# Performance work log

Hardware: AMD Instinct MI355X
Metric: run time of the kernel (lower is better)

## Reference

```python
import jax, jax.numpy as jnp
import numpy as np

D_MODEL, Q, V, H = 1024, 64, 64, 16
B, K = 2, 2048


def setup_inputs() -> dict:
    key = jax.random.key(0)
    ks = jax.random.split(key, 8)
    s = 0.02
    return {
        "xi": jax.random.normal(ks[0], (B, K, D_MODEL), dtype=jnp.float32),
        # stacked per-head projection weights (equivalent to h separate nn.Linear)
        "Wq": jax.random.normal(ks[1], (H, D_MODEL, Q), dtype=jnp.float32) * s,
        "bq": jax.random.normal(ks[2], (H, Q), dtype=jnp.float32) * s,
        "Wk": jax.random.normal(ks[3], (H, D_MODEL, Q), dtype=jnp.float32) * s,
        "bk": jax.random.normal(ks[4], (H, Q), dtype=jnp.float32) * s,
        "Wv": jax.random.normal(ks[5], (H, D_MODEL, V), dtype=jnp.float32) * s,
        "bv": jax.random.normal(ks[6], (H, V), dtype=jnp.float32) * s,
        "Wo": jax.random.normal(ks[7], (H * V, D_MODEL), dtype=jnp.float32) * s,
        "bo": jnp.zeros((D_MODEL,), dtype=jnp.float32),
    }


def reference(xi, Wq, bq, Wk, bk, Wv, bv, Wo, bo):
    # per-head projections, batched over heads: [B,H,K,q]
    queries = jnp.einsum("bkd,hdq->bhkq", xi, Wq) + bq[None, :, None, :]
    keys = jnp.einsum("bkd,hdq->bhkq", xi, Wk) + bk[None, :, None, :]
    values = jnp.einsum("bkd,hdv->bhkv", xi, Wv) + bv[None, :, None, :]
    # NOTE: original scales by sqrt(queries.shape[1]) == sqrt(seq_len K), not sqrt(q)
    scale = 1.0 / np.sqrt(xi.shape[1]).astype(np.float32)
    scores = jax.nn.softmax(jnp.einsum("bhkq,bhmq->bhkm", queries, keys) * scale, axis=-1)
    attn = jnp.einsum("bhkm,bhmv->bhkv", scores, values)  # [B,H,K,v]
    # concat heads along last dim -> [B,K,H*v]
    attn = attn.transpose(0, 2, 1, 3).reshape(xi.shape[0], xi.shape[1], -1)
    return attn @ Wo + bo
```

## Files before the change

kernel.cpp:

```cpp
#include <hip/hip_runtime.h>
#include <math.h>

typedef __bf16 bf16x8 __attribute__((ext_vector_type(8)));
typedef float  f32x4  __attribute__((ext_vector_type(4)));
typedef float  f32x16 __attribute__((ext_vector_type(16)));
typedef unsigned short u16x8 __attribute__((ext_vector_type(8)));

#define D_MODEL 1024
#define QDIM    64
#define HEADS   16
#define BATCH   2
#define SEQ     2048
#define M_ROWS  (BATCH*SEQ)
#define NCAT    (HEADS*3*QDIM)

__device__ __forceinline__ unsigned short f2bf(float f) {
    unsigned int u = __float_as_uint(f);
    u += 0x7fffu + ((u >> 16) & 1u);
    return (unsigned short)(u >> 16);
}

__device__ __forceinline__ void gl16(const unsigned short* g, unsigned short* l) {
    __builtin_amdgcn_global_load_lds(
        (const __attribute__((address_space(1))) unsigned int*)g,
        (__attribute__((address_space(3))) unsigned int*)l, 16, 0, 0);
}

__global__ __launch_bounds__(256) void k_cvt_bf16(const float* __restrict__ in,
                                                  unsigned short* __restrict__ out) {
    int i = (blockIdx.x * 256 + threadIdx.x) * 8;
    f32x4 a = *(const f32x4*)(in + i);
    f32x4 b = *(const f32x4*)(in + i + 4);
    u16x8 o;
    o[0]=f2bf(a[0]); o[1]=f2bf(a[1]); o[2]=f2bf(a[2]); o[3]=f2bf(a[3]);
    o[4]=f2bf(b[0]); o[5]=f2bf(b[1]); o[6]=f2bf(b[2]); o[7]=f2bf(b[3]);
    *(u16x8*)(out + i) = o;
}

__global__ __launch_bounds__(256) void k_prep_wcat(const float* __restrict__ Wq,
                                                   const float* __restrict__ Wk,
                                                   const float* __restrict__ Wv,
                                                   const float* __restrict__ bq,
                                                   const float* __restrict__ bk,
                                                   const float* __restrict__ bv,
                                                   unsigned short* __restrict__ WcatT,
                                                   float* __restrict__ bcat,
                                                   float qscale) {
    int blk = blockIdx.x;
    int dt = blk & 15, h = (blk >> 4) & 15, s = blk >> 8;
    const float* W = (s == 0) ? Wq : (s == 1) ? Wk : Wv;
    float sc = (s == 0) ? qscale : 1.0f;
    __shared__ float t[64][65];
    int tid = threadIdx.x;
    int dr = tid >> 2, qc = (tid & 3) * 16;
    const float* src = W + (size_t)h * (D_MODEL * QDIM) + (size_t)(dt * 64 + dr) * QDIM + qc;
#pragma unroll
    for (int j = 0; j < 4; ++j) {
        f32x4 v = *(const f32x4*)(src + j * 4);
        t[dr][qc + j * 4 + 0] = v[0]; t[dr][qc + j * 4 + 1] = v[1];
        t[dr][qc + j * 4 + 2] = v[2]; t[dr][qc + j * 4 + 3] = v[3];
    }
    __syncthreads();
    int q = tid >> 2, dc = (tid & 3) * 16;
    unsigned short* dst = WcatT + (size_t)(h * 192 + s * 64 + q) * D_MODEL + dt * 64 + dc;
#pragma unroll
    for (int j = 0; j < 2; ++j) {
        u16x8 o;
#pragma unroll
        for (int e = 0; e < 8; ++e) o[e] = f2bf(t[dc + j * 8 + e][q] * sc);
        *(u16x8*)(dst + j * 8) = o;
    }
    if (dt == 0 && tid < 64) {
        const float* bb = (s == 0) ? bq : (s == 1) ? bk : bv;
        bcat[h * 192 + s * 64 + tid] = bb[h * QDIM + tid] * sc;
    }
}

__global__ __launch_bounds__(256) void k_prep_wo(const float* __restrict__ Wo,
                                                 unsigned short* __restrict__ WoT) {
    int blk = blockIdx.x;
    int ct = blk & 15, rt = blk >> 4;
    __shared__ float t[64][65];
    int tid = threadIdx.x;
    int dr = tid >> 2, qc = (tid & 3) * 16;
    const float* src = Wo + (size_t)(rt * 64 + dr) * D_MODEL + ct * 64 + qc;
#pragma unroll
    for (int j = 0; j < 4; ++j) {
        f32x4 v = *(const f32x4*)(src + j * 4);
        t[dr][qc + j * 4 + 0] = v[0]; t[dr][qc + j * 4 + 1] = v[1];
        t[dr][qc + j * 4 + 2] = v[2]; t[dr][qc + j * 4 + 3] = v[3];
    }
    __syncthreads();
    int q = tid >> 2, dc = (tid & 3) * 16;
    unsigned short* dst = WoT + (size_t)(ct * 64 + q) * D_MODEL + rt * 64 + dc;
#pragma unroll
    for (int j = 0; j < 2; ++j) {
        u16x8 o;
#pragma unroll
        for (int e = 0; e < 8; ++e) o[e] = f2bf(t[dc + j * 8 + e][q]);
        *(u16x8*)(dst + j * 8) = o;
    }
}

template<bool OUT_BF16>
__global__ __launch_bounds__(256) void k_gemm(const unsigned short* __restrict__ A,
                                              const unsigned short* __restrict__ BT,
                                              const float* __restrict__ bias,
                                              void* __restrict__ Cout,
                                              int N, int Kd) {
    __shared__ __align__(16) unsigned short Alds[128 * 64];
    __shared__ __align__(16) unsigned short Blds[128 * 64];
    const int tid = threadIdx.x;
    const int lane = tid & 63, w = tid >> 6;
    const int g = lane >> 4, c = lane & 15;
    int nwg = gridDim.x * gridDim.y;
    int bid = blockIdx.y * gridDim.x + blockIdx.x;
    int sw = (bid & 7) * (nwg >> 3) + (bid >> 3);
    int bx = sw % gridDim.x, by = sw / gridDim.x;
    const int m0 = by * 128, n0 = bx * 128;
    const int wm = (w >> 1) * 64, wn = (w & 1) * 64;
    const int r8 = lane >> 3, chx = (lane & 7) ^ r8;
    const int swz = c & 7;
    f32x4 acc[4][4] = {};

    for (int k0 = 0; k0 < Kd; k0 += 64) {
        __builtin_amdgcn_sched_barrier(0);
        __builtin_amdgcn_s_barrier();
#pragma unroll
        for (int i = 0; i < 4; ++i) {
            int row = w * 32 + i * 8 + r8;
            gl16(A + (size_t)(m0 + row) * Kd + k0 + chx * 8, Alds + w * 2048 + i * 512);
            gl16(BT + (size_t)(n0 + row) * Kd + k0 + chx * 8, Blds + w * 2048 + i * 512);
        }
        asm volatile("s_waitcnt vmcnt(0)" ::: "memory");
        __builtin_amdgcn_s_barrier();
        __builtin_amdgcn_sched_barrier(0);
#pragma unroll
        for (int kk = 0; kk < 2; ++kk) {
            bf16x8 af[4], bfr[4];
#pragma unroll
            for (int mf = 0; mf < 4; ++mf) {
                int row = wm + mf * 16 + c;
                af[mf] = *(const bf16x8*)(Alds + row * 64 + (((kk * 4 + g) ^ swz) * 8));
            }
#pragma unroll
            for (int nf = 0; nf < 4; ++nf) {
                int row = wn + nf * 16 + c;
                bfr[nf] = *(const bf16x8*)(Blds + row * 64 + (((kk * 4 + g) ^ swz) * 8));
            }
            __builtin_amdgcn_s_setprio(1);
#pragma unroll
            for (int mf = 0; mf < 4; ++mf)
#pragma unroll
                for (int nf = 0; nf < 4; ++nf)
                    acc[mf][nf] = __builtin_amdgcn_mfma_f32_16x16x32_bf16(af[mf], bfr[nf], acc[mf][nf], 0, 0, 0);
            __builtin_amdgcn_s_setprio(0);
        }
    }

#pragma unroll
    for (int mf = 0; mf < 4; ++mf)
#pragma unroll
        for (int nf = 0; nf < 4; ++nf) {
            int col = n0 + wn + nf * 16 + c;
            float bb = bias[col];
#pragma unroll
            for (int r = 0; r < 4; ++r) {
                int row = m0 + wm + mf * 16 + 4 * g + r;
                float v = acc[mf][nf][r] + bb;
                if (OUT_BF16)
                    ((unsigned short*)Cout)[(size_t)row * N + col] = f2bf(v);
                else
                    ((float*)Cout)[(size_t)row * N + col] = v;
            }
        }
}

__global__ __launch_bounds__(256) void k_transpose_v(const unsigned short* __restrict__ qkv,
                                                     unsigned short* __restrict__ vt) {
    int blk = blockIdx.x;
    int kt = blk & 31, h = (blk >> 5) & 15, b = blk >> 9;
    __shared__ unsigned short t[64][72];
    int tid = threadIdx.x;
#pragma unroll
    for (int j = 0; j < 2; ++j) {
        int cid = tid + j * 256;
        int row = cid >> 3, ch = (cid & 7) * 8;
        *(u16x8*)&t[row][ch] =
            *(const u16x8*)(qkv + (size_t)(b * SEQ + kt * 64 + row) * NCAT + h * 192 + 128 + ch);
    }
    __syncthreads();
#pragma unroll
    for (int j = 0; j < 2; ++j) {
        int cid = tid + j * 256;
        int v = cid >> 3, ch = (cid & 7) * 8;
        u16x8 o;
#pragma unroll
        for (int e = 0; e < 8; ++e) o[e] = t[ch + e][v];
        *(u16x8*)(vt + (size_t)((b * HEADS + h) * QDIM + v) * SEQ + kt * 64 + ch) = o;
    }
}

__global__ __launch_bounds__(256) void k_attn(const unsigned short* __restrict__ qkv,
                                              const unsigned short* __restrict__ vt,
                                              unsigned short* __restrict__ attn) {
    int bid = blockIdx.x;
    int blk = (bid & 7) * 128 + (bid >> 3);
    int qt = blk & 31, h = (blk >> 5) & 15, b = blk >> 9;
    int tid = threadIdx.x, w = tid >> 6, lane = tid & 63;
    int l31 = lane & 31, hi = lane >> 5;
    int qh = w & 1, kh = w >> 1;

    __shared__ __align__(16) unsigned char KV[2][16384];

    const int qbase = b * SEQ + qt * 64;
    const unsigned short* qrow = qkv + (size_t)(qbase + qh * 32 + l31) * NCAT + h * 192;
    bf16x8 qf[4];
#pragma unroll
    for (int s = 0; s < 4; ++s) qf[s] = *(const bf16x8*)(qrow + s * 16 + hi * 8);

    f32x16 o0 = {}, o1 = {};
    float rsum = 0.f;

    const unsigned short* kg = qkv + (size_t)(b * SEQ) * NCAT + h * 192 + 64;
    const unsigned short* vg = vt + (size_t)((b * HEADS + h) * QDIM) * SEQ;

    const int r8 = lane >> 3, chx = (lane & 7) ^ r8;
    const int l7 = lane & 7;

    {
        unsigned short* kb = (unsigned short*)&KV[0][w * 2048];
        unsigned short* vb = (unsigned short*)&KV[0][8192 + w * 2048];
        gl16(kg + (size_t)(w * 16 + r8) * NCAT + chx * 8, kb);
        gl16(kg + (size_t)(w * 16 + 8 + r8) * NCAT + chx * 8, kb + 512);
        gl16(vg + (size_t)(w * 16 + r8) * SEQ + chx * 8, vb);
        gl16(vg + (size_t)(w * 16 + 8 + r8) * SEQ + chx * 8, vb + 512);
        asm volatile("s_waitcnt vmcnt(0)" ::: "memory");
    }
    __builtin_amdgcn_s_barrier();

    const int NT = SEQ / 64;
    for (int t = 0; t < NT; ++t) {
        const int cur = t & 1;
        if (t + 1 < NT) {
            const int t64 = (t + 1) * 64;
            unsigned short* kb = (unsigned short*)&KV[cur ^ 1][w * 2048];
            unsigned short* vb = (unsigned short*)&KV[cur ^ 1][8192 + w * 2048];
            gl16(kg + (size_t)(t64 + w * 16 + r8) * NCAT + chx * 8, kb);
            gl16(kg + (size_t)(t64 + w * 16 + 8 + r8) * NCAT + chx * 8, kb + 512);
            gl16(vg + (size_t)(w * 16 + r8) * SEQ + t64 + chx * 8, vb);
            gl16(vg + (size_t)(w * 16 + 8 + r8) * SEQ + t64 + chx * 8, vb + 512);
            asm volatile("s_waitcnt vmcnt(4)" ::: "memory");
        } else {
            asm volatile("s_waitcnt vmcnt(0)" ::: "memory");
        }
        __builtin_amdgcn_s_barrier();
        __builtin_amdgcn_sched_barrier(0);

        const unsigned char* Kl = &KV[cur][0];
        const unsigned char* Vl = &KV[cur][8192];

        f32x16 st = {};
        __builtin_amdgcn_s_setprio(1);
#pragma unroll
        for (int s = 0; s < 4; ++s) {
            int row = kh * 32 + l31;
            bf16x8 kf = *(const bf16x8*)(Kl + row * 128 + (((2 * s + hi) ^ l7) * 16));
            st = __builtin_amdgcn_mfma_f32_32x32x16_bf16(kf, qf[s], st, 0, 0, 0);
        }
        __builtin_amdgcn_s_setprio(0);

#pragma unroll
        for (int r = 0; r < 16; ++r) {
            float p = __expf(st[r]);
            st[r] = p;
            rsum += p;
        }
        unsigned int d0, d1, d2, d3, d4, d5, d6, d7;
        asm("v_cvt_pk_bf16_f32 %0, %1, %2" : "=v"(d0) : "v"(st[0]),  "v"(st[1]));
        asm("v_cvt_pk_bf16_f32 %0, %1, %2" : "=v"(d1) : "v"(st[2]),  "v"(st[3]));
        asm("v_cvt_pk_bf16_f32 %0, %1, %2" : "=v"(d2) : "v"(st[4]),  "v"(st[5]));
        asm("v_cvt_pk_bf16_f32 %0, %1, %2" : "=v"(d3) : "v"(st[6]),  "v"(st[7]));
        asm("v_cvt_pk_bf16_f32 %0, %1, %2" : "=v"(d4) : "v"(st[8]),  "v"(st[9]));
        asm("v_cvt_pk_bf16_f32 %0, %1, %2" : "=v"(d5) : "v"(st[10]), "v"(st[11]));
        asm("v_cvt_pk_bf16_f32 %0, %1, %2" : "=v"(d6) : "v"(st[12]), "v"(st[13]));
        asm("v_cvt_pk_bf16_f32 %0, %1, %2" : "=v"(d7) : "v"(st[14]), "v"(st[15]));
        asm("v_permlane32_swap_b32 %0, %1" : "+v"(d0), "+v"(d2));
        asm("v_permlane32_swap_b32 %0, %1" : "+v"(d1), "+v"(d3));
        asm("v_permlane32_swap_b32 %0, %1" : "+v"(d4), "+v"(d6));
        asm("v_permlane32_swap_b32 %0, %1" : "+v"(d5), "+v"(d7));
        union { unsigned int u[4]; bf16x8 v; } pa0, pa1;
        pa0.u[0] = d0; pa0.u[1] = d1; pa0.u[2] = d2; pa0.u[3] = d3;
        pa1.u[0] = d4; pa1.u[1] = d5; pa1.u[2] = d6; pa1.u[3] = d7;

        __builtin_amdgcn_s_setprio(1);
#pragma unroll
        for (int s = 0; s < 2; ++s) {
#pragma unroll
            for (int vh = 0; vh < 2; ++vh) {
                int row = vh * 32 + l31;
                bf16x8 vf = *(const bf16x8*)(Vl + row * 128 + (((kh * 4 + 2 * s + hi) ^ (row & 7)) * 16));
                if (vh == 0)
                    o0 = __builtin_amdgcn_mfma_f32_32x32x16_bf16(s ? pa1.v : pa0.v, vf, o0, 0, 0, 0);
                else
                    o1 = __builtin_amdgcn_mfma_f32_32x32x16_bf16(s ? pa1.v : pa0.v, vf, o1, 0, 0, 0);
            }
        }
        __builtin_amdgcn_s_setprio(0);
        __builtin_amdgcn_sched_barrier(0);
        __builtin_amdgcn_s_barrier();
    }

    rsum += __shfl_xor(rsum, 32);
    __syncthreads();
    float* red = (float*)&KV[0][0];
    float* rsb = (float*)&KV[1][0];
    if (kh == 1) {
#pragma unroll
        for (int r = 0; r < 16; ++r) {
            int q = (r & 3) + 8 * (r >> 2) + 4 * hi;
            red[(qh * 32 + q) * 64 + l31]      = o0[r];
            red[(qh * 32 + q) * 64 + 32 + l31] = o1[r];
        }
    }
    if (lane < 32) rsb[(kh * 2 + qh) * 32 + l31] = rsum;
    __syncthreads();
    if (kh == 0) {
#pragma unroll
        for (int r = 0; r < 16; ++r) {
            int q = (r & 3) + 8 * (r >> 2) + 4 * hi;
            float tot = rsb[qh * 32 + q] + rsb[(2 + qh) * 32 + q];
            float inv = 1.0f / tot;
            float v0 = (o0[r] + red[(qh * 32 + q) * 64 + l31]) * inv;
            float v1 = (o1[r] + red[(qh * 32 + q) * 64 + 32 + l31]) * inv;
            int row = qbase + qh * 32 + q;
            attn[(size_t)row * (HEADS * QDIM) + h * QDIM + l31]      = f2bf(v0);
            attn[(size_t)row * (HEADS * QDIM) + h * QDIM + 32 + l31] = f2bf(v1);
        }
    }
}

extern "C" void kernel_launch(void* const* d_in, const int* in_sizes, int n_in,
                              void* d_out, int out_size, void* d_ws, size_t ws_size,
                              hipStream_t stream) {
    const float* xi = (const float*)d_in[0];
    const float* Wq = (const float*)d_in[1];
    const float* bq = (const float*)d_in[2];
    const float* Wk = (const float*)d_in[3];
    const float* bk = (const float*)d_in[4];
    const float* Wv = (const float*)d_in[5];
    const float* bv = (const float*)d_in[6];
    const float* Wo = (const float*)d_in[7];
    const float* bo = (const float*)d_in[8];

    unsigned short* xi_bf = (unsigned short*)d_ws;
    unsigned short* WcatT = xi_bf + (size_t)M_ROWS * D_MODEL;
    unsigned short* WoT   = WcatT + (size_t)NCAT * D_MODEL;
    float*          bcat  = (float*)(WoT + (size_t)D_MODEL * D_MODEL);
    unsigned short* qkvc  = (unsigned short*)(bcat + NCAT);
    unsigned short* vtb   = qkvc + (size_t)M_ROWS * NCAT;
    unsigned short* attnb = vtb + (size_t)BATCH * HEADS * QDIM * SEQ;

    float qscale = 1.0f / sqrtf((float)SEQ);

    k_cvt_bf16<<<(M_ROWS * D_MODEL) / 2048, 256, 0, stream>>>(xi, xi_bf);
    k_prep_wcat<<<768, 256, 0, stream>>>(Wq, Wk, Wv, bq, bk, bv, WcatT, bcat, qscale);
    k_prep_wo<<<256, 256, 0, stream>>>(Wo, WoT);

    k_gemm<true><<<dim3(NCAT / 128, M_ROWS / 128), 256, 0, stream>>>(
        xi_bf, WcatT, bcat, (void*)qkvc, NCAT, D_MODEL);

    k_transpose_v<<<BATCH * HEADS * (SEQ / 64), 256, 0, stream>>>(qkvc, vtb);

    k_attn<<<BATCH * HEADS * (SEQ / 64), 256, 0, stream>>>(qkvc, vtb, attnb);

    k_gemm<false><<<dim3(D_MODEL / 128, M_ROWS / 128), 256, 0, stream>>>(
        attnb, WoT, bo, d_out, D_MODEL, D_MODEL);
}
```

Measured before the change: 135.6 us.

## Stage K/V tiles in MFMA fragment order and use exp2 with folded log2e

```diff
diff --git a/kernel.cpp b/kernel.cpp
--- a/kernel.cpp
+++ b/kernel.cpp
@@ -225,31 +225,37 @@
     const unsigned short* kg = qkv + (size_t)(b * SEQ) * NCAT + h * 192 + 64;
     const unsigned short* vg = vt + (size_t)((b * HEADS + h) * QDIM) * SEQ;
 
-    const int r8 = lane >> 3, chx = (lane & 7) ^ r8;
-    const int l7 = lane & 7;
-
+    const unsigned short* ks0; const unsigned short* ks1;
+    const unsigned short* vs0; const unsigned short* vs1;
+    unsigned kd0, kd1, vd0, vd1;
     {
-        unsigned short* kb = (unsigned short*)&KV[0][w * 2048];
-        unsigned short* vb = (unsigned short*)&KV[0][8192 + w * 2048];
-        gl16(kg + (size_t)(w * 16 + r8) * NCAT + chx * 8, kb);
-        gl16(kg + (size_t)(w * 16 + 8 + r8) * NCAT + chx * 8, kb + 512);
-        gl16(vg + (size_t)(w * 16 + r8) * SEQ + chx * 8, vb);
-        gl16(vg + (size_t)(w * 16 + 8 + r8) * SEQ + chx * 8, vb + 512);
-        asm volatile("s_waitcnt vmcnt(0)" ::: "memory");
-    }
+        int f0 = w, f1 = w + 4;
+        ks0 = kg + (size_t)((f0 >> 2) * 32 + l31) * NCAT + (f0 & 3) * 16 + hi * 8;
+        ks1 = kg + (size_t)((f1 >> 2) * 32 + l31) * NCAT + (f1 & 3) * 16 + hi * 8;
+        kd0 = f0 * 1024; kd1 = f1 * 1024;
+        vs0 = vg + (size_t)((f0 & 1) * 32 + l31) * SEQ + (f0 >> 2) * 32 + ((f0 >> 1) & 1) * 16 + hi * 8;
+        vs1 = vg + (size_t)((f1 & 1) * 32 + l31) * SEQ + (f1 >> 2) * 32 + ((f1 >> 1) & 1) * 16 + hi * 8;
+        vd0 = 8192 + f0 * 1024; vd1 = 8192 + f1 * 1024;
+    }
+    const int lx = lane * 16;
+
+    gl16(ks0, (unsigned short*)&KV[0][kd0]);
+    gl16(vs0, (unsigned short*)&KV[0][vd0]);
+    gl16(ks1, (unsigned short*)&KV[0][kd1]);
+    gl16(vs1, (unsigned short*)&KV[0][vd1]);
+    ks0 += 64 * NCAT; ks1 += 64 * NCAT; vs0 += 64; vs1 += 64;
+    asm volatile("s_waitcnt vmcnt(0)" ::: "memory");
     __builtin_amdgcn_s_barrier();
 
     const int NT = SEQ / 64;
     for (int t = 0; t < NT; ++t) {
         const int cur = t & 1;
         if (t + 1 < NT) {
-            const int t64 = (t + 1) * 64;
-            unsigned short* kb = (unsigned short*)&KV[cur ^ 1][w * 2048];
-            unsigned short* vb = (unsigned short*)&KV[cur ^ 1][8192 + w * 2048];
-            gl16(kg + (size_t)(t64 + w * 16 + r8) * NCAT + chx * 8, kb);
-            gl16(kg + (size_t)(t64 + w * 16 + 8 + r8) * NCAT + chx * 8, kb + 512);
-            gl16(vg + (size_t)(w * 16 + r8) * SEQ + t64 + chx * 8, vb);
-            gl16(vg + (size_t)(w * 16 + 8 + r8) * SEQ + t64 + chx * 8, vb + 512);
+            gl16(ks0, (unsigned short*)&KV[cur ^ 1][kd0]);
+            gl16(vs0, (unsigned short*)&KV[cur ^ 1][vd0]);
+            gl16(ks1, (unsigned short*)&KV[cur ^ 1][kd1]);
+            gl16(vs1, (unsigned short*)&KV[cur ^ 1][vd1]);
+            ks0 += 64 * NCAT; ks1 += 64 * NCAT; vs0 += 64; vs1 += 64;
             asm volatile("s_waitcnt vmcnt(4)" ::: "memory");
         } else {
             asm volatile("s_waitcnt vmcnt(0)" ::: "memory");
@@ -257,22 +263,21 @@
         __builtin_amdgcn_s_barrier();
         __builtin_amdgcn_sched_barrier(0);
 
-        const unsigned char* Kl = &KV[cur][0];
-        const unsigned char* Vl = &KV[cur][8192];
+        const unsigned char* Kf = &KV[cur][0];
+        const unsigned char* Vf = &KV[cur][8192];
 
         f32x16 st = {};
         __builtin_amdgcn_s_setprio(1);
 #pragma unroll
         for (int s = 0; s < 4; ++s) {
-            int row = kh * 32 + l31;
-            bf16x8 kf = *(const bf16x8*)(Kl + row * 128 + (((2 * s + hi) ^ l7) * 16));
+            bf16x8 kf = *(const bf16x8*)(Kf + (kh * 4 + s) * 1024 + lx);
             st = __builtin_amdgcn_mfma_f32_32x32x16_bf16(kf, qf[s], st, 0, 0, 0);
         }
         __builtin_amdgcn_s_setprio(0);
 
 #pragma unroll
         for (int r = 0; r < 16; ++r) {
-            float p = __expf(st[r]);
+            float p = __builtin_amdgcn_exp2f(st[r]);
             st[r] = p;
             rsum += p;
         }
@@ -294,17 +299,15 @@
         pa1.u[0] = d4; pa1.u[1] = d5; pa1.u[2] = d6; pa1.u[3] = d7;
 
         __builtin_amdgcn_s_setprio(1);
-#pragma unroll
-        for (int s = 0; s < 2; ++s) {
-#pragma unroll
-            for (int vh = 0; vh < 2; ++vh) {
-                int row = vh * 32 + l31;
-                bf16x8 vf = *(const bf16x8*)(Vl + row * 128 + (((kh * 4 + 2 * s + hi) ^ (row & 7)) * 16));
-                if (vh == 0)
-                    o0 = __builtin_amdgcn_mfma_f32_32x32x16_bf16(s ? pa1.v : pa0.v, vf, o0, 0, 0, 0);
-                else
-                    o1 = __builtin_amdgcn_mfma_f32_32x32x16_bf16(s ? pa1.v : pa0.v, vf, o1, 0, 0, 0);
-            }
+        {
+            bf16x8 vf00 = *(const bf16x8*)(Vf + (kh * 4 + 0) * 1024 + lx);
+            bf16x8 vf01 = *(const bf16x8*)(Vf + (kh * 4 + 1) * 1024 + lx);
+            bf16x8 vf10 = *(const bf16x8*)(Vf + (kh * 4 + 2) * 1024 + lx);
+            bf16x8 vf11 = *(const bf16x8*)(Vf + (kh * 4 + 3) * 1024 + lx);
+            o0 = __builtin_amdgcn_mfma_f32_32x32x16_bf16(pa0.v, vf00, o0, 0, 0, 0);
+            o1 = __builtin_amdgcn_mfma_f32_32x32x16_bf16(pa0.v, vf01, o1, 0, 0, 0);
+            o0 = __builtin_amdgcn_mfma_f32_32x32x16_bf16(pa1.v, vf10, o0, 0, 0, 0);
+            o1 = __builtin_amdgcn_mfma_f32_32x32x16_bf16(pa1.v, vf11, o1, 0, 0, 0);
         }
         __builtin_amdgcn_s_setprio(0);
         __builtin_amdgcn_sched_barrier(0);
@@ -361,7 +364,7 @@
     unsigned short* vtb   = qkvc + (size_t)M_ROWS * NCAT;
     unsigned short* attnb = vtb + (size_t)BATCH * HEADS * QDIM * SEQ;
 
-    float qscale = 1.0f / sqrtf((float)SEQ);
+    float qscale = 1.4426950408889634f / sqrtf((float)SEQ);
 
     k_cvt_bf16<<<(M_ROWS * D_MODEL) / 2048, 256, 0, stream>>>(xi, xi_bf);
     k_prep_wcat<<<768, 256, 0, stream>>>(Wq, Wk, Wv, bq, bk, bv, WcatT, bcat, qscale);
```

After: 145.9 us. 1.08x slower.
